# Performance work log

Hardware: AMD Instinct MI355X
Metric: run time of the kernel (lower is better)

Reference implementation:

```python
import jax, jax.numpy as jnp
import numpy as np
from jax import lax

B, T, D, H, L = 128, 512, 256, 256, 2


def setup_inputs() -> dict:
    key = jax.random.key(0)
    ks = jax.random.split(key, 8)
    s = 1.0 / np.sqrt(H)
    return {
        "input1": jax.random.normal(ks[0], (B, T, D), jnp.float32),
        "input2": jax.random.normal(ks[1], (B, T, D), jnp.float32),
        "W_ih": jax.random.normal(ks[2], (L, 4 * H, D), jnp.float32) * s,
        "W_hh": jax.random.normal(ks[3], (L, 4 * H, H), jnp.float32) * s,
        "b_ih": jax.random.normal(ks[4], (L, 4 * H), jnp.float32) * s,
        "b_hh": jax.random.normal(ks[5], (L, 4 * H), jnp.float32) * s,
        "fc_w": jax.random.normal(ks[6], (5, H), jnp.float32) * s,
        "fc_b": jax.random.normal(ks[7], (5,), jnp.float32) * s,
    }


def _lstm_layer(x, Wih, Whh, bih, bhh):
    # x: [B, T, in]; returns (outputs [B, T, H], final h [B, H])
    b = x.shape[0]
    # precompute input projection for all timesteps (one big GEMM)
    xg = jnp.einsum('bti,gi->btg', x, Wih) + bih + bhh  # [B, T, 4H]
    h0 = jnp.zeros((b, H), x.dtype)
    c0 = jnp.zeros((b, H), x.dtype)

    def step(carry, xg_t):
        h, c = carry
        gates = xg_t + h @ Whh.T  # [B, 4H]
        i, f, g, o = jnp.split(gates, 4, axis=-1)
        i = jax.nn.sigmoid(i)
        f = jax.nn.sigmoid(f)
        g = jnp.tanh(g)
        o = jax.nn.sigmoid(o)
        c = f * c + i * g
        h = o * jnp.tanh(c)
        return (h, c), h

    (h_last, _), hs = lax.scan(step, (h0, c0), jnp.swapaxes(xg, 0, 1))
    return jnp.swapaxes(hs, 0, 1), h_last


def _forward_once(x, W_ih, W_hh, b_ih, b_hh, fc_w, fc_b):
    h_finals = []
    out = x
    for l in range(L):
        out, h_last = _lstm_layer(out, W_ih[l], W_hh[l], b_ih[l], b_hh[l])
        h_finals.append(h_last)
    hn = jnp.stack(h_finals, axis=0).reshape(-1, H)  # [L*B, H] (torch hn.view)
    return jax.nn.relu(hn) @ fc_w.T + fc_b  # [L*B, 5]


def reference(input1, input2, W_ih, W_hh, b_ih, b_hh, fc_w, fc_b):
    out1 = _forward_once(input1, W_ih, W_hh, b_ih, b_hh, fc_w, fc_b)
    out2 = _forward_once(input2, W_ih, W_hh, b_ih, b_hh, fc_w, fc_b)
    return (out1, out2)
```

## Files before the change

### kernel.cpp

```cpp
#include <hip/hip_runtime.h>
#include <hip/hip_fp16.h>

typedef unsigned int  u32;
typedef unsigned short u16;

typedef _Float16 h2v __attribute__((ext_vector_type(2)));
typedef _Float16 h8v __attribute__((ext_vector_type(8)));
typedef float    f4v __attribute__((ext_vector_type(4)));

static __device__ __forceinline__ u16 f2h_bits(float x){
    _Float16 h = (_Float16)x;
    return __builtin_bit_cast(u16, h);
}
static __device__ __forceinline__ u32 pack2(float a, float b){
    return (u32)f2h_bits(a) | ((u32)f2h_bits(b) << 16);
}
static __device__ __forceinline__ float fdot2(u32 w, u32 h, float acc){
#if __has_builtin(__builtin_amdgcn_fdot2)
    return __builtin_amdgcn_fdot2(__builtin_bit_cast(h2v, w),
                                  __builtin_bit_cast(h2v, h), acc, false);
#else
    h2v wv = __builtin_bit_cast(h2v, w), hv = __builtin_bit_cast(h2v, h);
    return acc + (float)wv[0]*(float)hv[0] + (float)wv[1]*(float)hv[1];
#endif
}
template<int CTRL>
static __device__ __forceinline__ float dpp_qp(float x){
#if __has_builtin(__builtin_amdgcn_mov_dpp)
    int r = __builtin_amdgcn_mov_dpp(__builtin_bit_cast(int, x), CTRL, 0xF, 0xF, true);
    return __builtin_bit_cast(float, r);
#else
    return __shfl_xor(x, (CTRL == 0xB1) ? 1 : 2);
#endif
}


__global__ void cvt_weights(const float* __restrict__ Wih,
                            const float* __restrict__ Whh,
                            const float* __restrict__ bih,
                            const float* __restrict__ bhh,
                            u32* __restrict__ wih16u,
                            u32* __restrict__ wreg,
                            u32* __restrict__ wldsg,
                            float* __restrict__ bias){
    u32 e = blockIdx.x * blockDim.x + threadIdx.x;
    {
        float2 v = ((const float2*)Wih)[e];
        wih16u[e] = pack2(v.x, v.y);
    }
    if (e < 196608u){
        u32 l = (e >= 98304u) ? 1u : 0u;
        u32 rem = e - l*98304u;
        u32 pidx = rem >> 10, L = rem & 1023u;
        u32 r = pidx / 24u, p = pidx - r*24u;
        u32 j = L >> 2, q = L & 3u;
        u32 row = r*256u + j;
        u32 P = 32u*q + p;
        float2 v = ((const float2*)Whh)[((size_t)l*1024u + row)*128u + P];
        wreg[e] = pack2(v.x, v.y);
    } else {
        u32 e2 = e - 196608u;
        u32 l = e2 >> 15, rem = e2 & 32767u;
        u32 i2 = rem >> 10, L = rem & 1023u;
        u32 r = i2 >> 3, k = i2 & 7u;
        u32 j = L >> 2, q = L & 3u;
        u32 row = r*256u + j;
        u32 P = 32u*q + 24u + k;
        float2 v = ((const float2*)Whh)[((size_t)l*1024u + row)*128u + P];
        wldsg[e2] = pack2(v.x, v.y);
    }
    if (e < 2048u){
        u32 l = e >> 10, Ls = e & 1023u;
        u32 src = l*1024u + (((Ls & 3u) << 8) | (Ls >> 2));
        bias[e] = bih[src] + bhh[src];
    }
}

__global__ void cvt_chunk(const float* __restrict__ in1,
                          const float* __restrict__ in2,
                          u16* __restrict__ a16,
                          int t0, int lgTc){
    u32 idx = blockIdx.x * blockDim.x + threadIdx.x;
    u32 c4  = idx & 63;
    u32 row = idx >> 6;
    u32 tc   = row & ((1u << lgTc) - 1u);
    u32 beta = row >> lgTc;
    const float* base = (beta < 128u) ? in1 : in2;
    float4 v = *(const float4*)(base + ((size_t)(beta & 127u)*512u + (size_t)(t0 + tc))*256u + c4*4u);
    ((uint2*)a16)[idx] = make_uint2(pack2(v.x, v.y), pack2(v.z, v.w));
}

#define MPW 4
__global__ __launch_bounds__(256) void proj_gemm(
        const u16*  __restrict__ A16,
        const u16*  __restrict__ Bw,
        u16*        __restrict__ Cout){
    __shared__ u16 Blds[128][264];
    const int tid = threadIdx.x;
    const int n0 = blockIdx.y * 128;

    {
        const uint4* src = (const uint4*)Bw;
        #pragma unroll
        for (int i = 0; i < 16; i++){
            int idx = i*256 + tid;
            int r = idx >> 5, c4 = idx & 31;
            uint4 v = src[(size_t)(n0 + r)*32 + c4];
            *(uint4*)&Blds[r][c4*8] = v;
        }
    }
    __syncthreads();

    const int l   = tid & 63;
    const int wid = tid >> 6;
    const int wm = (wid >> 1) * 64;
    const int wn = (wid & 1) * 64;
    const int lr = l & 15;
    const int lk = l >> 4;

    for (int mt = 0; mt < MPW; mt++){
        const int m0 = (blockIdx.x*MPW + mt) * 128;

        f4v acc[4][4] = {};
        const u16* a16p[4];
        #pragma unroll
        for (int f = 0; f < 4; f++)
            a16p[f] = A16 + (size_t)(m0 + wm + f*16 + lr)*256 + lk*8;

        #pragma unroll
        for (int ks = 0; ks < 8; ks++){
            uint4 a_[4], b_[4];
            #pragma unroll
            for (int f = 0; f < 4; f++)
                a_[f] = *(const uint4*)(a16p[f] + ks*32);
            #pragma unroll
            for (int f = 0; f < 4; f++)
                b_[f] = *(const uint4*)&Blds[wn + f*16 + lr][ks*32 + lk*8];
            #pragma unroll
            for (int fm = 0; fm < 4; fm++)
                #pragma unroll
                for (int fn = 0; fn < 4; fn++)
                    acc[fm][fn] = __builtin_amdgcn_mfma_f32_16x16x32_f16(
                        __builtin_bit_cast(h8v, a_[fm]),
                        __builtin_bit_cast(h8v, b_[fn]),
                        acc[fm][fn], 0, 0, 0);
        }

        #pragma unroll
        for (int fm = 0; fm < 4; fm++){
            #pragma unroll
            for (int i = 0; i < 4; i++){
                int m = m0 + wm + fm*16 + lk*4 + i;
                size_t rowoff = (size_t)m*1024;
                #pragma unroll
                for (int fn = 0; fn < 4; fn++){
                    int n = n0 + wn + fn*16 + lr;
                    int np = ((n & 255) << 2) | (n >> 8);
                    Cout[rowoff + np] = f2h_bits(acc[fm][fn][i]);
                }
            }
        }
    }
}

__global__ __launch_bounds__(1024, 4) void lstm_rec(
        const u16* __restrict__ xg,
        const u32* __restrict__ wreg,
        const u32* __restrict__ wldsg,
        const float* __restrict__ bias,
        u16* __restrict__ hseq,
        u16* __restrict__ h_state,
        float* __restrict__ c_state,
        int Tc, int write_seq, int first){
    __shared__ u32 wlds[1024*36];
    __shared__ alignas(16) u16 hbufF[2*288];

    const int L    = threadIdx.x;
    const int q    = L & 3;
    const int j    = L >> 2;
    const int beta = blockIdx.x;

    u32 w[96];
    #pragma unroll
    for (int t = 0; t < 96; t++)
        w[t] = wreg[(size_t)t*1024 + L];
    #pragma unroll
    for (int i = 0; i < 32; i++)
        wlds[L*36 + i] = wldsg[(size_t)i*1024 + L];

    const float bs = bias[L];
    float c = 0.f;
    u16 hb_last = 0;
    if (q == 0){
        u16 h0 = first ? (u16)0 : h_state[(size_t)beta*256 + j];
        hbufF[72*(j >> 6) + (j & 63)] = h0;
        hb_last = h0;
        if (!first) c = c_state[(size_t)beta*256 + j];
    }
    __syncthreads();

    const u16* xr = xg + (size_t)beta * Tc * 1024 + L;
    u16 xcur = xr[0];
    const uint4* wr = (const uint4*)&wlds[L*36];

    #pragma unroll 2
    for (int tc = 0; tc < Tc; tc++){
        u16 xnext = xr[(size_t)(tc+1)*1024];

        const uint4* hv = (const uint4*)&hbufF[(tc & 1)*288 + 72*q];
        float pA = 0.f, pB = 0.f, pC = 0.f, pD = 0.f;

        #pragma unroll
        for (int i = 0; i < 6; i++){
            uint4 hh = hv[i];
            pA = fdot2(w[   4*i+0], hh.x, pA); pA = fdot2(w[   4*i+1], hh.y, pA);
            pA = fdot2(w[   4*i+2], hh.z, pA); pA = fdot2(w[   4*i+3], hh.w, pA);
            pB = fdot2(w[24+4*i+0], hh.x, pB); pB = fdot2(w[24+4*i+1], hh.y, pB);
            pB = fdot2(w[24+4*i+2], hh.z, pB); pB = fdot2(w[24+4*i+3], hh.w, pB);
            pC = fdot2(w[48+4*i+0], hh.x, pC); pC = fdot2(w[48+4*i+1], hh.y, pC);
            pC = fdot2(w[48+4*i+2], hh.z, pC); pC = fdot2(w[48+4*i+3], hh.w, pC);
            pD = fdot2(w[72+4*i+0], hh.x, pD); pD = fdot2(w[72+4*i+1], hh.y, pD);
            pD = fdot2(w[72+4*i+2], hh.z, pD); pD = fdot2(w[72+4*i+3], hh.w, pD);
        }
        #pragma unroll
        for (int m = 0; m < 2; m++){
            uint4 hh = hv[6+m];
            uint4 wa = wr[0+m], wb = wr[2+m], wc = wr[4+m], wd = wr[6+m];
            pA = fdot2(wa.x, hh.x, pA); pA = fdot2(wa.y, hh.y, pA);
            pA = fdot2(wa.z, hh.z, pA); pA = fdot2(wa.w, hh.w, pA);
            pB = fdot2(wb.x, hh.x, pB); pB = fdot2(wb.y, hh.y, pB);
            pB = fdot2(wb.z, hh.z, pB); pB = fdot2(wb.w, hh.w, pB);
            pC = fdot2(wc.x, hh.x, pC); pC = fdot2(wc.y, hh.y, pC);
            pC = fdot2(wc.z, hh.z, pC); pC = fdot2(wc.w, hh.w, pC);
            pD = fdot2(wd.x, hh.x, pD); pD = fdot2(wd.y, hh.y, pD);
            pD = fdot2(wd.z, hh.z, pD); pD = fdot2(wd.w, hh.w, pD);
        }

        float k0_ = (q & 1) ? pB : pA;
        float k1_ = (q & 1) ? pD : pC;
        float s0_ = (q & 1) ? pA : pB;
        float s1_ = (q & 1) ? pC : pD;
        k0_ += dpp_qp<0xB1>(s0_);
        k1_ += dpp_qp<0xB1>(s1_);
        float kf = (q & 2) ? k1_ : k0_;
        float sf = (q & 2) ? k0_ : k1_;
        kf += dpp_qp<0x4E>(sf);

        float acc = kf + bs + (float)__builtin_bit_cast(_Float16, xcur);

        float targ = (q == 2) ? 2.f*acc : -acc;
        float e1 = __expf(targ);
        float rr = 1.f / (1.f + e1);
        float a  = (q == 2) ? 1.f - 2.f*rr : rr;

        float p1 = dpp_qp<0xB1>(a);
        float p2 = dpp_qp<0x4E>(a);
        float p3 = dpp_qp<0x4E>(p1);

        c = (q == 0) ? (p1*c + a*p2) : 0.f;
        float e2 = __expf(2.f*c);
        float th = 1.f - 2.f/(e2 + 1.f);
        float h  = p3 * th;
        u16 hb = f2h_bits(h);

        if (q == 0){
            hbufF[((tc & 1)^1)*288 + 72*(j >> 6) + (j & 63)] = hb;
            hb_last = hb;
            if (write_seq) hseq[((size_t)beta*Tc + tc)*256 + j] = hb;
        }
        xcur = xnext;
        __syncthreads();
    }

    if (q == 0){
        h_state[(size_t)beta*256 + j] = hb_last;
        c_state[(size_t)beta*256 + j] = c;
    }
}

__global__ void fc_out(const u16* __restrict__ hlast,
                       const float* __restrict__ fcw,
                       const float* __restrict__ fcb,
                       float* __restrict__ out){
    int r = blockIdx.x;
    int lane = threadIdx.x;
    int inp = r >> 8, rem = r & 255, l = rem >> 7, b = rem & 127;
    int beta = inp*128 + b;
    const u16* h = hlast + ((size_t)l*256 + beta)*256;

    int j0 = lane * 4;
    uint2 hb = *(const uint2*)(h + j0);
    h2v p0 = __builtin_bit_cast(h2v, hb.x), p1 = __builtin_bit_cast(h2v, hb.y);
    float hv0 = fmaxf((float)p0[0], 0.f);
    float hv1 = fmaxf((float)p0[1], 0.f);
    float hv2 = fmaxf((float)p1[0], 0.f);
    float hv3 = fmaxf((float)p1[1], 0.f);

    float acc[5];
    #pragma unroll
    for (int k = 0; k < 5; k++){
        float4 w = *(const float4*)(fcw + k*256 + j0);
        acc[k] = hv0*w.x + hv1*w.y + hv2*w.z + hv3*w.w;
    }
    #pragma unroll
    for (int k = 0; k < 5; k++)
        #pragma unroll
        for (int off = 32; off > 0; off >>= 1)
            acc[k] += __shfl_xor(acc[k], off);
    if (lane == 0){
        #pragma unroll
        for (int k = 0; k < 5; k++)
            out[(size_t)r*5 + k] = acc[k] + fcb[k];
    }
}

extern "C" void kernel_launch(void* const* d_in, const int* in_sizes, int n_in,
                              void* d_out, int out_size, void* d_ws, size_t ws_size,
                              hipStream_t stream) {
    const float* in1 = (const float*)d_in[0];
    const float* in2 = (const float*)d_in[1];
    const float* Wih = (const float*)d_in[2];
    const float* Whh = (const float*)d_in[3];
    const float* bih = (const float*)d_in[4];
    const float* bhh = (const float*)d_in[5];
    const float* fcw = (const float*)d_in[6];
    const float* fcb = (const float*)d_in[7];
    float* out = (float*)d_out;

    char* ws = (char*)d_ws;
    u16*   wih16   = (u16*)  (ws + 0x000000);
    u32*   wreg    = (u32*)  (ws + 0x100000);
    u32*   wldsg   = (u32*)  (ws + 0x1C0000);
    float* bias    = (float*)(ws + 0x200000);
    u16*   h_state = (u16*)  (ws + 0x202000);
    float* c_state = (float*)(ws + 0x242000);
    const size_t chunk_off = 0x300000;

    int Tc = 8;
    for (int cand = 512; cand >= 8; cand >>= 1){
        if (chunk_off + (size_t)cand * 655360ull <= ws_size){ Tc = cand; break; }
    }
    int lgTc = 31 - __builtin_clz((u32)Tc);
    u16* xgc = (u16*)(ws + chunk_off);
    u16* hsc = (u16*)(ws + chunk_off + (size_t)Tc * 524288ull);

    cvt_weights<<<1024, 256, 0, stream>>>(Wih, Whh, bih, bhh,
                                          (u32*)wih16, wreg, wldsg, bias);

    const int nch = 512 / Tc;
    dim3 pg(2*Tc/MPW, 8);
    for (int k = 0; k < nch; k++){
        int t0 = k * Tc;
        cvt_chunk<<<64*Tc, 256, 0, stream>>>(in1, in2, hsc, t0, lgTc);
        proj_gemm<<<pg, 256, 0, stream>>>(hsc, wih16, xgc);
        lstm_rec<<<256, 1024, 0, stream>>>((const u16*)xgc, wreg, wldsg, bias,
                                           hsc, h_state, c_state,
                                           Tc, 1, k == 0);
        proj_gemm<<<pg, 256, 0, stream>>>(hsc, wih16 + 262144, xgc);
        lstm_rec<<<256, 1024, 0, stream>>>((const u16*)xgc, wreg + 98304, wldsg + 32768,
                                           bias + 1024,
                                           (u16*)nullptr, h_state + 65536, c_state + 65536,
                                           Tc, 0, k == 0);
    }
    fc_out<<<512, 64, 0, stream>>>(h_state, fcw, fcb, out);
}
```

Measured before the change: 2.287 ms.

## Process two batch sequences per LSTM recurrence block to reuse register weights

Each recurrent block now advances two independent sequences (beta and beta+128) at once, so each weight register and LDS weight load is reused for two hidden-state dot products. The grid halves from 256 to 128 blocks, which cuts the per-block weight loading and amortises the per-step barrier and activation latency over twice the work. The cost is more registers for the second set of accumulators, possible spills under the 1024-thread launch bounds, and only 128 blocks for 256 CUs, leaving half the CUs idle.

```diff
diff --git a/kernel.cpp b/kernel.cpp
--- a/kernel.cpp
+++ b/kernel.cpp
@@ -14,6 +14,9 @@
 }
 static __device__ __forceinline__ u32 pack2(float a, float b){
     return (u32)f2h_bits(a) | ((u32)f2h_bits(b) << 16);
+}
+static __device__ __forceinline__ float h2f(u16 b){
+    return (float)__builtin_bit_cast(_Float16, b);
 }
 static __device__ __forceinline__ float fdot2(u32 w, u32 h, float acc){
 #if __has_builtin(__builtin_amdgcn_fdot2)
@@ -173,12 +176,13 @@
         float* __restrict__ c_state,
         int Tc, int write_seq, int first){
     __shared__ u32 wlds[1024*36];
-    __shared__ alignas(16) u16 hbufF[2*288];
+    __shared__ alignas(16) u16 hbufF[2*2*288];
 
     const int L    = threadIdx.x;
     const int q    = L & 3;
     const int j    = L >> 2;
-    const int beta = blockIdx.x;
+    const int beta0 = blockIdx.x;
+    const int beta1 = blockIdx.x + 128;
 
     u32 w[96];
     #pragma unroll
@@ -189,92 +193,142 @@
         wlds[L*36 + i] = wldsg[(size_t)i*1024 + L];
 
     const float bs = bias[L];
-    float c = 0.f;
-    u16 hb_last = 0;
+    float c0 = 0.f, c1 = 0.f;
+    u16 hbl0 = 0, hbl1 = 0;
     if (q == 0){
-        u16 h0 = first ? (u16)0 : h_state[(size_t)beta*256 + j];
-        hbufF[72*(j >> 6) + (j & 63)] = h0;
-        hb_last = h0;
-        if (!first) c = c_state[(size_t)beta*256 + j];
+        int off = 72*(j >> 6) + (j & 63);
+        u16 h00 = first ? (u16)0 : h_state[(size_t)beta0*256 + j];
+        u16 h01 = first ? (u16)0 : h_state[(size_t)beta1*256 + j];
+        hbufF[off] = h00;  hbufF[288 + off] = h01;
+        hbl0 = h00; hbl1 = h01;
+        if (!first){
+            c0 = c_state[(size_t)beta0*256 + j];
+            c1 = c_state[(size_t)beta1*256 + j];
+        }
     }
     __syncthreads();
 
-    const u16* xr = xg + (size_t)beta * Tc * 1024 + L;
-    u16 xcur = xr[0];
+    const u16* xr0 = xg + (size_t)beta0 * Tc * 1024 + L;
+    const u16* xr1 = xg + (size_t)beta1 * Tc * 1024 + L;
+    u16 xc0 = xr0[0], xc1 = xr1[0];
     const uint4* wr = (const uint4*)&wlds[L*36];
 
     #pragma unroll 2
     for (int tc = 0; tc < Tc; tc++){
-        u16 xnext = xr[(size_t)(tc+1)*1024];
-
-        const uint4* hv = (const uint4*)&hbufF[(tc & 1)*288 + 72*q];
-        float pA = 0.f, pB = 0.f, pC = 0.f, pD = 0.f;
+        u16 xn0 = xr0[(size_t)(tc+1)*1024];
+        u16 xn1 = xr1[(size_t)(tc+1)*1024];
+
+        const uint4* hv0 = (const uint4*)&hbufF[(tc & 1)*576 + 72*q];
+        const uint4* hv1 = (const uint4*)&hbufF[(tc & 1)*576 + 288 + 72*q];
+        float pA0 = 0.f, pB0 = 0.f, pC0 = 0.f, pD0 = 0.f;
+        float pA1 = 0.f, pB1 = 0.f, pC1 = 0.f, pD1 = 0.f;
 
         #pragma unroll
         for (int i = 0; i < 6; i++){
-            uint4 hh = hv[i];
-            pA = fdot2(w[   4*i+0], hh.x, pA); pA = fdot2(w[   4*i+1], hh.y, pA);
-            pA = fdot2(w[   4*i+2], hh.z, pA); pA = fdot2(w[   4*i+3], hh.w, pA);
-            pB = fdot2(w[24+4*i+0], hh.x, pB); pB = fdot2(w[24+4*i+1], hh.y, pB);
-            pB = fdot2(w[24+4*i+2], hh.z, pB); pB = fdot2(w[24+4*i+3], hh.w, pB);
-            pC = fdot2(w[48+4*i+0], hh.x, pC); pC = fdot2(w[48+4*i+1], hh.y, pC);
-            pC = fdot2(w[48+4*i+2], hh.z, pC); pC = fdot2(w[48+4*i+3], hh.w, pC);
-            pD = fdot2(w[72+4*i+0], hh.x, pD); pD = fdot2(w[72+4*i+1], hh.y, pD);
-            pD = fdot2(w[72+4*i+2], hh.z, pD); pD = fdot2(w[72+4*i+3], hh.w, pD);
+            uint4 h0 = hv0[i], h1 = hv1[i];
+            pA0 = fdot2(w[   4*i+0], h0.x, pA0); pA1 = fdot2(w[   4*i+0], h1.x, pA1);
+            pA0 = fdot2(w[   4*i+1], h0.y, pA0); pA1 = fdot2(w[   4*i+1], h1.y, pA1);
+            pA0 = fdot2(w[   4*i+2], h0.z, pA0); pA1 = fdot2(w[   4*i+2], h1.z, pA1);
+            pA0 = fdot2(w[   4*i+3], h0.w, pA0); pA1 = fdot2(w[   4*i+3], h1.w, pA1);
+            pB0 = fdot2(w[24+4*i+0], h0.x, pB0); pB1 = fdot2(w[24+4*i+0], h1.x, pB1);
+            pB0 = fdot2(w[24+4*i+1], h0.y, pB0); pB1 = fdot2(w[24+4*i+1], h1.y, pB1);
+            pB0 = fdot2(w[24+4*i+2], h0.z, pB0); pB1 = fdot2(w[24+4*i+2], h1.z, pB1);
+            pB0 = fdot2(w[24+4*i+3], h0.w, pB0); pB1 = fdot2(w[24+4*i+3], h1.w, pB1);
+            pC0 = fdot2(w[48+4*i+0], h0.x, pC0); pC1 = fdot2(w[48+4*i+0], h1.x, pC1);
+            pC0 = fdot2(w[48+4*i+1], h0.y, pC0); pC1 = fdot2(w[48+4*i+1], h1.y, pC1);
+            pC0 = fdot2(w[48+4*i+2], h0.z, pC0); pC1 = fdot2(w[48+4*i+2], h1.z, pC1);
+            pC0 = fdot2(w[48+4*i+3], h0.w, pC0); pC1 = fdot2(w[48+4*i+3], h1.w, pC1);
+            pD0 = fdot2(w[72+4*i+0], h0.x, pD0); pD1 = fdot2(w[72+4*i+0], h1.x, pD1);
+            pD0 = fdot2(w[72+4*i+1], h0.y, pD0); pD1 = fdot2(w[72+4*i+1], h1.y, pD1);
+            pD0 = fdot2(w[72+4*i+2], h0.z, pD0); pD1 = fdot2(w[72+4*i+2], h1.z, pD1);
+            pD0 = fdot2(w[72+4*i+3], h0.w, pD0); pD1 = fdot2(w[72+4*i+3], h1.w, pD1);
         }
         #pragma unroll
         for (int m = 0; m < 2; m++){
-            uint4 hh = hv[6+m];
+            uint4 h0 = hv0[6+m], h1 = hv1[6+m];
             uint4 wa = wr[0+m], wb = wr[2+m], wc = wr[4+m], wd = wr[6+m];
-            pA = fdot2(wa.x, hh.x, pA); pA = fdot2(wa.y, hh.y, pA);
-            pA = fdot2(wa.z, hh.z, pA); pA = fdot2(wa.w, hh.w, pA);
-            pB = fdot2(wb.x, hh.x, pB); pB = fdot2(wb.y, hh.y, pB);
-            pB = fdot2(wb.z, hh.z, pB); pB = fdot2(wb.w, hh.w, pB);
-            pC = fdot2(wc.x, hh.x, pC); pC = fdot2(wc.y, hh.y, pC);
-            pC = fdot2(wc.z, hh.z, pC); pC = fdot2(wc.w, hh.w, pC);
-            pD = fdot2(wd.x, hh.x, pD); pD = fdot2(wd.y, hh.y, pD);
-            pD = fdot2(wd.z, hh.z, pD); pD = fdot2(wd.w, hh.w, pD);
-        }
-
-        float k0_ = (q & 1) ? pB : pA;
-        float k1_ = (q & 1) ? pD : pC;
-        float s0_ = (q & 1) ? pA : pB;
-        float s1_ = (q & 1) ? pC : pD;
-        k0_ += dpp_qp<0xB1>(s0_);
-        k1_ += dpp_qp<0xB1>(s1_);
-        float kf = (q & 2) ? k1_ : k0_;
-        float sf = (q & 2) ? k0_ : k1_;
-        kf += dpp_qp<0x4E>(sf);
-
-        float acc = kf + bs + (float)__builtin_bit_cast(_Float16, xcur);
-
-        float targ = (q == 2) ? 2.f*acc : -acc;
-        float e1 = __expf(targ);
-        float rr = 1.f / (1.f + e1);
-        float a  = (q == 2) ? 1.f - 2.f*rr : rr;
-
-        float p1 = dpp_qp<0xB1>(a);
-        float p2 = dpp_qp<0x4E>(a);
-        float p3 = dpp_qp<0x4E>(p1);
-
-        c = (q == 0) ? (p1*c + a*p2) : 0.f;
-        float e2 = __expf(2.f*c);
-        float th = 1.f - 2.f/(e2 + 1.f);
-        float h  = p3 * th;
-        u16 hb = f2h_bits(h);
+            pA0 = fdot2(wa.x, h0.x, pA0); pA1 = fdot2(wa.x, h1.x, pA1);
+            pA0 = fdot2(wa.y, h0.y, pA0); pA1 = fdot2(wa.y, h1.y, pA1);
+            pA0 = fdot2(wa.z, h0.z, pA0); pA1 = fdot2(wa.z, h1.z, pA1);
+            pA0 = fdot2(wa.w, h0.w, pA0); pA1 = fdot2(wa.w, h1.w, pA1);
+            pB0 = fdot2(wb.x, h0.x, pB0); pB1 = fdot2(wb.x, h1.x, pB1);
+            pB0 = fdot2(wb.y, h0.y, pB0); pB1 = fdot2(wb.y, h1.y, pB1);
+            pB0 = fdot2(wb.z, h0.z, pB0); pB1 = fdot2(wb.z, h1.z, pB1);
+            pB0 = fdot2(wb.w, h0.w, pB0); pB1 = fdot2(wb.w, h1.w, pB1);
+            pC0 = fdot2(wc.x, h0.x, pC0); pC1 = fdot2(wc.x, h1.x, pC1);
+            pC0 = fdot2(wc.y, h0.y, pC0); pC1 = fdot2(wc.y, h1.y, pC1);
+            pC0 = fdot2(wc.z, h0.z, pC0); pC1 = fdot2(wc.z, h1.z, pC1);
+            pC0 = fdot2(wc.w, h0.w, pC0); pC1 = fdot2(wc.w, h1.w, pC1);
+            pD0 = fdot2(wd.x, h0.x, pD0); pD1 = fdot2(wd.x, h1.x, pD1);
+            pD0 = fdot2(wd.y, h0.y, pD0); pD1 = fdot2(wd.y, h1.y, pD1);
+            pD0 = fdot2(wd.z, h0.z, pD0); pD1 = fdot2(wd.z, h1.z, pD1);
+            pD0 = fdot2(wd.w, h0.w, pD0); pD1 = fdot2(wd.w, h1.w, pD1);
+        }
+
+        float ka0 = (q & 1) ? pB0 : pA0;
+        float kb0 = (q & 1) ? pD0 : pC0;
+        float sa0 = (q & 1) ? pA0 : pB0;
+        float sb0 = (q & 1) ? pC0 : pD0;
+        ka0 += dpp_qp<0xB1>(sa0);
+        kb0 += dpp_qp<0xB1>(sb0);
+        float kf0 = (q & 2) ? kb0 : ka0;
+        float sf0 = (q & 2) ? ka0 : kb0;
+        kf0 += dpp_qp<0x4E>(sf0);
+        float acc0 = kf0 + bs + h2f(xc0);
+        float ka1 = (q & 1) ? pB1 : pA1;
+        float kb1 = (q & 1) ? pD1 : pC1;
+        float sa1 = (q & 1) ? pA1 : pB1;
+        float sb1 = (q & 1) ? pC1 : pD1;
+        ka1 += dpp_qp<0xB1>(sa1);
+        kb1 += dpp_qp<0xB1>(sb1);
+        float kf1 = (q & 2) ? kb1 : ka1;
+        float sf1 = (q & 2) ? ka1 : kb1;
+        kf1 += dpp_qp<0x4E>(sf1);
+        float acc1 = kf1 + bs + h2f(xc1);
+
+        float targ0 = (q == 2) ? 2.f*acc0 : -acc0;
+        float targ1 = (q == 2) ? 2.f*acc1 : -acc1;
+        float e10 = __expf(targ0);
+        float e11 = __expf(targ1);
+        float rr0 = 1.f / (1.f + e10);
+        float rr1 = 1.f / (1.f + e11);
+        float a0 = (q == 2) ? 1.f - 2.f*rr0 : rr0;
+        float a1 = (q == 2) ? 1.f - 2.f*rr1 : rr1;
+
+        float p10 = dpp_qp<0xB1>(a0);
+        float p20 = dpp_qp<0x4E>(a0);
+        float p30 = dpp_qp<0x4E>(p10);
+        float p11 = dpp_qp<0xB1>(a1);
+        float p21 = dpp_qp<0x4E>(a1);
+        float p31 = dpp_qp<0x4E>(p11);
+
+        c0 = (q == 0) ? (p10*c0 + a0*p20) : 0.f;
+        c1 = (q == 0) ? (p11*c1 + a1*p21) : 0.f;
+        float e20 = __expf(2.f*c0);
+        float e21 = __expf(2.f*c1);
+        float th0 = 1.f - 2.f/(e20 + 1.f);
+        float th1 = 1.f - 2.f/(e21 + 1.f);
+        u16 hb0 = f2h_bits(p30 * th0);
+        u16 hb1 = f2h_bits(p31 * th1);
 
         if (q == 0){
-            hbufF[((tc & 1)^1)*288 + 72*(j >> 6) + (j & 63)] = hb;
-            hb_last = hb;
-            if (write_seq) hseq[((size_t)beta*Tc + tc)*256 + j] = hb;
-        }
-        xcur = xnext;
+            int off = ((tc & 1)^1)*576 + 72*(j >> 6) + (j & 63);
+            hbufF[off] = hb0;  hbufF[288 + off] = hb1;
+            hbl0 = hb0; hbl1 = hb1;
+            if (write_seq){
+                hseq[((size_t)beta0*Tc + tc)*256 + j] = hb0;
+                hseq[((size_t)beta1*Tc + tc)*256 + j] = hb1;
+            }
+        }
+        xc0 = xn0; xc1 = xn1;
         __syncthreads();
     }
 
     if (q == 0){
-        h_state[(size_t)beta*256 + j] = hb_last;
-        c_state[(size_t)beta*256 + j] = c;
+        h_state[(size_t)beta0*256 + j] = hbl0;
+        h_state[(size_t)beta1*256 + j] = hbl1;
+        c_state[(size_t)beta0*256 + j] = c0;
+        c_state[(size_t)beta1*256 + j] = c1;
     }
 }
 
@@ -353,11 +407,11 @@
         int t0 = k * Tc;
         cvt_chunk<<<64*Tc, 256, 0, stream>>>(in1, in2, hsc, t0, lgTc);
         proj_gemm<<<pg, 256, 0, stream>>>(hsc, wih16, xgc);
-        lstm_rec<<<256, 1024, 0, stream>>>((const u16*)xgc, wreg, wldsg, bias,
+        lstm_rec<<<128, 1024, 0, stream>>>((const u16*)xgc, wreg, wldsg, bias,
                                            hsc, h_state, c_state,
                                            Tc, 1, k == 0);
         proj_gemm<<<pg, 256, 0, stream>>>(hsc, wih16 + 262144, xgc);
-        lstm_rec<<<256, 1024, 0, stream>>>((const u16*)xgc, wreg + 98304, wldsg + 32768,
+        lstm_rec<<<128, 1024, 0, stream>>>((const u16*)xgc, wreg + 98304, wldsg + 32768,
                                            bias + 1024,
                                            (u16*)nullptr, h_state + 65536, c_state + 65536,
                                            Tc, 0, k == 0);
```

Measured after the change: 4.097 ms. 1.79x slower.
